# Kernel optimization log

Measured on AMD Instinct MI355X. Metric: run time of the kernel, lower is better.

The kernel has to match this reference:

```python
import jax, jax.numpy as jnp
import numpy as np

E, K, H, I = 16, 4, 2048, 1024
B, S = 1, 2048


def setup_inputs() -> dict:
    key = jax.random.key(0)
    ks = jax.random.split(key, 5)
    scale_in = 1.0 / np.sqrt(H)
    scale_mid = 1.0 / np.sqrt(I)
    return {
        "x": jax.random.normal(ks[0], (B, S, H), dtype=jnp.float32),
        "gate_w": jax.random.normal(ks[1], (E, H), dtype=jnp.float32) * scale_in,
        "w1_gate": jax.random.normal(ks[2], (E, I, H), dtype=jnp.float32) * scale_in,
        "w1_up": jax.random.normal(ks[3], (E, I, H), dtype=jnp.float32) * scale_in,
        "w2": jax.random.normal(ks[4], (E, H, I), dtype=jnp.float32) * scale_mid,
        "topk": K,
    }


def reference(x, gate_w, w1_gate, w1_up, w2, topk):
    orig_shape = x.shape
    xt = x.reshape(-1, x.shape[-1])            # [T, H]
    T = xt.shape[0]
    n_exp = gate_w.shape[0]

    # Router: top-k logits, softmax over the selected k (as in the torch code).
    logits = xt @ gate_w.T                      # [T, E]
    topk_vals, topk_ids = jax.lax.top_k(logits, topk)
    topk_w = jax.nn.softmax(topk_vals, axis=-1)  # [T, K]

    # Dense per-token-per-expert combine weight; 0 for unselected experts.
    # Mathematically identical to the gather/scatter-add loop: unselected
    # experts contribute expert_out * 0.
    gate_dense = jnp.zeros((T, n_exp), dtype=xt.dtype)
    gate_dense = gate_dense.at[jnp.arange(T)[:, None], topk_ids].add(topk_w)

    # SwiGLU per expert (dense over experts; weights zero-out unused ones).
    g = jnp.einsum("th,eih->tei", xt, w1_gate)   # [T, E, I]
    u = jnp.einsum("th,eih->tei", xt, w1_up)     # [T, E, I]
    h = jax.nn.silu(g) * u                        # [T, E, I]
    out = jnp.einsum("tei,te,ehi->th", h, gate_dense, w2)  # [T, H]
    return out.reshape(orig_shape)
```

## Files before the change

### kernel.cpp

```cpp
#include <hip/hip_runtime.h>
#include <hip/hip_bf16.h>
#include <stdint.h>

#define NEXP 16
#define KSEL 4
#define HDIM 2048
#define IDIM 1024
#define TTOK 2048
#define MAXTILES 80
#define NTA 8
#define NTB 16
#define MAXBA (MAXTILES * NTA)
#define MAXBB (MAXTILES * NTB)
#define NCVT 1024
#define NW8 ((NEXP * IDIM * HDIM) / 8)

typedef __attribute__((ext_vector_type(8))) short bf16x8;
typedef __attribute__((ext_vector_type(4))) float f32x4;
typedef __attribute__((ext_vector_type(4))) unsigned int u32x4;
typedef unsigned int u32;

__device__ __forceinline__ uint32_t pack2(float a, float b) {
  __hip_bfloat162 h = __float22bfloat162_rn(float2{a, b});
  uint32_t u;
  __builtin_memcpy(&u, &h, 4);
  return u;
}
__device__ __forceinline__ ushort bf1(float a) {
  __hip_bfloat16 h = __float2bfloat16(a);
  ushort u;
  __builtin_memcpy(&u, &h, 2);
  return u;
}
__device__ __forceinline__ float bf2f(ushort u) {
  uint32_t v = (uint32_t)u << 16;
  float f;
  __builtin_memcpy(&f, &v, 4);
  return f;
}
__device__ __forceinline__ void gload16(const void* g, void* l) {
  __builtin_amdgcn_global_load_lds(
      (const __attribute__((address_space(1))) u32*)g,
      (__attribute__((address_space(3))) u32*)l, 16, 0, 0);
}
__device__ __forceinline__ int swzread(int row, int q) {
  return row * 32 + ((q ^ ((row >> 1) & 3)) << 3);
}
__device__ __forceinline__ void cvt_body(const float* __restrict__ src,
                                         ushort* __restrict__ dst,
                                         int blk, int nblk) {
  const int stride = nblk * 256;
  for (int i = blk * 256 + (int)threadIdx.x; i < NW8; i += stride) {
    f32x4 a = __builtin_nontemporal_load(((const f32x4*)src) + i * 2);
    f32x4 b = __builtin_nontemporal_load(((const f32x4*)src) + i * 2 + 1);
    uint4 t;
    t.x = pack2(a[0], a[1]); t.y = pack2(a[2], a[3]);
    t.z = pack2(b[0], b[1]); t.w = pack2(b[2], b[3]);
    ((uint4*)dst)[i] = t;
  }
}

__global__ __launch_bounds__(256) void router_kernel(
    const float* __restrict__ x, const float* __restrict__ gw,
    ushort* __restrict__ xb, int* __restrict__ topk_id,
    float* __restrict__ topk_w,
    const float* __restrict__ srcG, ushort* __restrict__ dstG,
    const float* __restrict__ srcU, ushort* __restrict__ dstU)
{
  if (blockIdx.x >= TTOK / 4 + NCVT) {
    cvt_body(srcU, dstU, blockIdx.x - (TTOK / 4 + NCVT), NCVT);
    return;
  }
  if (blockIdx.x >= TTOK / 4) {
    cvt_body(srcG, dstG, blockIdx.x - TTOK / 4, NCVT);
    return;
  }
  const int wid = threadIdx.x >> 6;
  const int lane = threadIdx.x & 63;
  const int t = blockIdx.x * 4 + wid;
  const float4* x4 = (const float4*)(x + (size_t)t * HDIM);
  const float4* gw4 = (const float4*)gw;
  float acc[NEXP];
#pragma unroll
  for (int e = 0; e < NEXP; ++e) acc[e] = 0.f;
#pragma unroll
  for (int i = 0; i < HDIM / 256; ++i) {
    const int idx = i * 64 + lane;
    float4 xv = x4[idx];
    uint2 xp;
    xp.x = pack2(xv.x, xv.y);
    xp.y = pack2(xv.z, xv.w);
    *(uint2*)(xb + (size_t)t * HDIM + idx * 4) = xp;
#pragma unroll
    for (int e = 0; e < NEXP; ++e) {
      float4 wv = gw4[e * (HDIM / 4) + idx];
      acc[e] += xv.x * wv.x + xv.y * wv.y + xv.z * wv.z + xv.w * wv.w;
    }
  }
#pragma unroll
  for (int e = 0; e < NEXP; ++e) {
#pragma unroll
    for (int off = 32; off >= 1; off >>= 1)
      acc[e] += __shfl_xor(acc[e], off);
  }
  if (lane == 0) {
    unsigned taken = 0;
    float vals[KSEL];
    int ids[KSEL];
#pragma unroll
    for (int k = 0; k < KSEL; ++k) {
      float bv = -3.4e38f; int bi = 0;
      for (int e = 0; e < NEXP; ++e)
        if (!((taken >> e) & 1u) && acc[e] > bv) { bv = acc[e]; bi = e; }
      taken |= 1u << bi; vals[k] = bv; ids[k] = bi;
    }
    float m = vals[0], s = 0.f, w[KSEL];
#pragma unroll
    for (int k = 0; k < KSEL; ++k) { w[k] = __expf(vals[k] - m); s += w[k]; }
    float is = 1.f / s;
#pragma unroll
    for (int k = 0; k < KSEL; ++k) {
      topk_id[t * KSEL + k] = ids[k];
      topk_w[t * KSEL + k] = w[k] * is;
    }
  }
}

__global__ __launch_bounds__(1024) void plan_scatter_kernel(
    const int* __restrict__ topk_id, int* __restrict__ counts,
    int* __restrict__ offsets, int* __restrict__ nWA, int* __restrict__ nWB,
    int* __restrict__ wlA, int* __restrict__ wlB,
    int* __restrict__ rowTok, int* __restrict__ inv)
{
  __shared__ int cnt[NEXP], off[NEXP], cur[NEXP], tiles[NEXP], pre[NEXP];
  const int tid = threadIdx.x;
  if (tid < NEXP) { cnt[tid] = 0; cur[tid] = 0; }
  __syncthreads();
  for (int i = tid; i < TTOK * KSEL; i += 1024)
    atomicAdd(&cnt[topk_id[i]], 1);
  __syncthreads();
  if (tid == 0) {
    int s = 0, p = 0;
    for (int e = 0; e < NEXP; ++e) {
      off[e] = s; s += cnt[e];
      tiles[e] = (cnt[e] + 127) >> 7;
      pre[e] = p; p += tiles[e];
    }
    *nWA = p * NTA;
    *nWB = p * NTB;
  }
  __syncthreads();
  if (tid < NEXP) {
    counts[tid] = cnt[tid];
    offsets[tid] = off[tid];
    const int e = tid, T = tiles[e];
    int idx = pre[e] * NTA;
    for (int nt = 0; nt < NTA; ++nt)
      for (int mt = 0; mt < T; ++mt)
        wlA[idx++] = (e << 12) | (nt << 6) | mt;
  } else if (tid < 2 * NEXP) {
    const int e = tid - NEXP, T = tiles[e];
    int idx = pre[e] * NTB;
    for (int nt = 0; nt < NTB; ++nt)
      for (int mt = 0; mt < T; ++mt)
        wlB[idx++] = (e << 12) | (nt << 6) | mt;
  }
  for (int i = tid; i < TTOK * KSEL; i += 1024) {
    const int e = topk_id[i];
    const int pos = atomicAdd(&cur[e], 1);
    const int row = off[e] + pos;
    rowTok[row] = i >> 2;
    inv[i] = row;
  }
}

__global__ __launch_bounds__(256) void gemmA_kernel(
    const ushort* __restrict__ xb,
    const ushort* __restrict__ wG, ushort* __restrict__ gbuf,
    const ushort* __restrict__ wU, ushort* __restrict__ ubuf,
    const int* __restrict__ rowTok, const int* __restrict__ counts,
    const int* __restrict__ offsets, const int* __restrict__ nW,
    const int* __restrict__ wl,
    const float* __restrict__ cvsrc, ushort* __restrict__ cvdst)
{
  int bid = blockIdx.x;
  if (bid >= 2 * MAXBA) {
    cvt_body(cvsrc, cvdst, bid - 2 * MAXBA, NCVT);
    return;
  }
  const ushort* wb;
  ushort* outb;
  if (bid >= MAXBA) { wb = wU; outb = ubuf; bid -= MAXBA; }
  else              { wb = wG; outb = gbuf; }

  const int nTot = *nW;
  const int L = (bid & 7) * (MAXBA / 8) + (bid >> 3);
  if (L >= nTot) return;
  const int w = wl[L];
  const int e = w >> 12, nt = (w >> 6) & 63, mt = w & 63;
  const int n_e = counts[e], rowbase = offsets[e];

  __shared__ ushort As[2][128 * 32];
  __shared__ ushort Bs[2][128 * 32];

  const int tid = threadIdx.x;
  const int r0 = tid >> 2;
  const int ck = tid & 3;
  const int sch = (ck ^ ((r0 >> 1) & 3)) << 3;

  const int ar0 = mt * 128 + r0, ar1 = ar0 + 64;
  const int tok0 = rowTok[rowbase + (ar0 < n_e ? ar0 : n_e - 1)];
  const int tok1 = rowTok[rowbase + (ar1 < n_e ? ar1 : n_e - 1)];
  const ushort* pA0 = xb + (size_t)tok0 * HDIM + sch;
  const ushort* pA1 = xb + (size_t)tok1 * HDIM + sch;
  const size_t wbase = (size_t)e * IDIM * HDIM;
  const ushort* pB0 = wb + wbase + (size_t)(nt * 128 + r0) * HDIM + sch;
  const ushort* pB1 = wb + wbase + (size_t)(nt * 128 + r0 + 64) * HDIM + sch;

  const int lane = tid & 63;
  const int wid = tid >> 6;
  const int wr = (wid >> 1) << 6;
  const int wc = (wid & 1) << 6;
  const int lr = lane & 15;
  const int q = lane >> 4;

  f32x4 acc[4][4];
#pragma unroll
  for (int i = 0; i < 4; ++i)
#pragma unroll
    for (int j = 0; j < 4; ++j) acc[i][j] = (f32x4){0.f, 0.f, 0.f, 0.f};

  auto STAGE = [&](int b) {
    gload16(pA0, &As[b][tid * 8]);
    gload16(pA1, &As[b][2048 + tid * 8]);
    gload16(pB0, &Bs[b][tid * 8]);
    gload16(pB1, &Bs[b][2048 + tid * 8]);
    pA0 += 32; pA1 += 32; pB0 += 32; pB1 += 32;
  };

  const int NTK = HDIM / 32;
  STAGE(0);
  __syncthreads();
  int buf = 0;
  for (int kt = 0; kt < NTK; ++kt) {
    if (kt + 1 < NTK) STAGE(buf ^ 1);
    bf16x8 af[4], bfr[4];
#pragma unroll
    for (int mi = 0; mi < 4; ++mi)
      af[mi] = *(const bf16x8*)&As[buf][swzread(wr + mi * 16 + lr, q)];
#pragma unroll
    for (int ni = 0; ni < 4; ++ni)
      bfr[ni] = *(const bf16x8*)&Bs[buf][swzread(wc + ni * 16 + lr, q)];
#pragma unroll
    for (int mi = 0; mi < 4; ++mi)
#pragma unroll
      for (int ni = 0; ni < 4; ++ni)
        acc[mi][ni] = __builtin_amdgcn_mfma_f32_16x16x32_bf16(af[mi], bfr[ni], acc[mi][ni], 0, 0, 0);
    __syncthreads();
    buf ^= 1;
  }

#pragma unroll
  for (int mi = 0; mi < 4; ++mi) {
#pragma unroll
    for (int ni = 0; ni < 4; ++ni) {
      const int col = nt * 128 + wc + ni * 16 + lr;
#pragma unroll
      for (int r = 0; r < 4; ++r) {
        const int mrow = mt * 128 + wr + mi * 16 + q * 4 + r;
        if (mrow < n_e)
          outb[(size_t)(rowbase + mrow) * IDIM + col] = bf1(acc[mi][ni][r]);
      }
    }
  }
}

__global__ __launch_bounds__(256) void gemmB_kernel(
    const ushort* __restrict__ hb, const ushort* __restrict__ wb,
    const int* __restrict__ counts, const int* __restrict__ offsets,
    const int* __restrict__ nW, const int* __restrict__ wl,
    ushort* __restrict__ po)
{
  const int nTot = *nW;
  const int L = (blockIdx.x & 7) * (MAXBB / 8) + (blockIdx.x >> 3);
  if (L >= nTot) return;
  const int w = wl[L];
  const int e = w >> 12, nt = (w >> 6) & 63, mt = w & 63;
  const int n_e = counts[e], rowbase = offsets[e];

  __shared__ ushort As[2][128 * 32];
  __shared__ ushort Bs[2][128 * 32];

  const int tid = threadIdx.x;
  const int r0 = tid >> 2;
  const int ck = tid & 3;
  const int sch = (ck ^ ((r0 >> 1) & 3)) << 3;

  const int ar0 = mt * 128 + r0, ar1 = ar0 + 64;
  const int g0 = rowbase + (ar0 < n_e ? ar0 : n_e - 1);
  const int g1 = rowbase + (ar1 < n_e ? ar1 : n_e - 1);
  const ushort* pA0 = hb + (size_t)g0 * IDIM + sch;
  const ushort* pA1 = hb + (size_t)g1 * IDIM + sch;
  const size_t wbase = (size_t)e * HDIM * IDIM;
  const ushort* pB0 = wb + wbase + (size_t)(nt * 128 + r0) * IDIM + sch;
  const ushort* pB1 = wb + wbase + (size_t)(nt * 128 + r0 + 64) * IDIM + sch;

  const int lane = tid & 63;
  const int wid = tid >> 6;
  const int wr = (wid >> 1) << 6;
  const int wc = (wid & 1) << 6;
  const int lr = lane & 15;
  const int q = lane >> 4;

  f32x4 acc[4][4];
#pragma unroll
  for (int i = 0; i < 4; ++i)
#pragma unroll
    for (int j = 0; j < 4; ++j) acc[i][j] = (f32x4){0.f, 0.f, 0.f, 0.f};

  auto STAGE = [&](int b) {
    gload16(pA0, &As[b][tid * 8]);
    gload16(pA1, &As[b][2048 + tid * 8]);
    gload16(pB0, &Bs[b][tid * 8]);
    gload16(pB1, &Bs[b][2048 + tid * 8]);
    pA0 += 32; pA1 += 32; pB0 += 32; pB1 += 32;
  };

  const int NTK = IDIM / 32;
  STAGE(0);
  __syncthreads();
  int buf = 0;
  for (int kt = 0; kt < NTK; ++kt) {
    if (kt + 1 < NTK) STAGE(buf ^ 1);
    bf16x8 af[4], bfr[4];
#pragma unroll
    for (int mi = 0; mi < 4; ++mi)
      af[mi] = *(const bf16x8*)&As[buf][swzread(wr + mi * 16 + lr, q)];
#pragma unroll
    for (int ni = 0; ni < 4; ++ni)
      bfr[ni] = *(const bf16x8*)&Bs[buf][swzread(wc + ni * 16 + lr, q)];
#pragma unroll
    for (int mi = 0; mi < 4; ++mi)
#pragma unroll
      for (int ni = 0; ni < 4; ++ni)
        acc[mi][ni] = __builtin_amdgcn_mfma_f32_16x16x32_bf16(af[mi], bfr[ni], acc[mi][ni], 0, 0, 0);
    __syncthreads();
    buf ^= 1;
  }

#pragma unroll
  for (int mi = 0; mi < 4; ++mi) {
#pragma unroll
    for (int ni = 0; ni < 4; ++ni) {
      const int col = nt * 128 + wc + ni * 16 + lr;
#pragma unroll
      for (int r = 0; r < 4; ++r) {
        const int mrow = mt * 128 + wr + mi * 16 + q * 4 + r;
        if (mrow < n_e)
          po[(size_t)(rowbase + mrow) * HDIM + col] = bf1(acc[mi][ni][r]);
      }
    }
  }
}

__global__ __launch_bounds__(256) void silu_kernel(
    const ushort* __restrict__ g, const ushort* __restrict__ u,
    ushort* __restrict__ h, int n8)
{
  const int stride = gridDim.x * 256;
  for (int i = blockIdx.x * 256 + threadIdx.x; i < n8; i += stride) {
    u32x4 gv = __builtin_nontemporal_load(((const u32x4*)g) + i);
    u32x4 uv = __builtin_nontemporal_load(((const u32x4*)u) + i);
    uint4 hv;
#pragma unroll
    for (int wd = 0; wd < 4; ++wd) {
      const uint32_t gw2 = gv[wd], uw2 = uv[wd];
      const float g0 = bf2f((ushort)(gw2 & 0xffff));
      const float g1 = bf2f((ushort)(gw2 >> 16));
      const float u0 = bf2f((ushort)(uw2 & 0xffff));
      const float u1 = bf2f((ushort)(uw2 >> 16));
      const float h0 = (g0 / (1.f + __expf(-g0))) * u0;
      const float h1 = (g1 / (1.f + __expf(-g1))) * u1;
      (&hv.x)[wd] = pack2(h0, h1);
    }
    ((uint4*)h)[i] = hv;
  }
}

__global__ __launch_bounds__(256) void combine_kernel(
    const ushort* __restrict__ po, const int* __restrict__ inv,
    const float* __restrict__ tw, float* __restrict__ out)
{
  const int t = blockIdx.x;
  const int r0 = inv[t * 4 + 0], r1 = inv[t * 4 + 1];
  const int r2 = inv[t * 4 + 2], r3 = inv[t * 4 + 3];
  const float w0 = tw[t * 4 + 0], w1 = tw[t * 4 + 1];
  const float w2v = tw[t * 4 + 2], w3 = tw[t * 4 + 3];
  const int i = threadIdx.x;
  uint4 v0 = *(const uint4*)(po + (size_t)r0 * HDIM + i * 8);
  uint4 v1 = *(const uint4*)(po + (size_t)r1 * HDIM + i * 8);
  uint4 v2 = *(const uint4*)(po + (size_t)r2 * HDIM + i * 8);
  uint4 v3 = *(const uint4*)(po + (size_t)r3 * HDIM + i * 8);
  float o[8];
#pragma unroll
  for (int w = 0; w < 4; ++w) {
    const uint32_t a = (&v0.x)[w], b = (&v1.x)[w], c = (&v2.x)[w], d = (&v3.x)[w];
    o[w * 2 + 0] = w0 * __builtin_bit_cast(float, a << 16) +
                   w1 * __builtin_bit_cast(float, b << 16) +
                   w2v * __builtin_bit_cast(float, c << 16) +
                   w3 * __builtin_bit_cast(float, d << 16);
    o[w * 2 + 1] = w0 * __builtin_bit_cast(float, a & 0xffff0000u) +
                   w1 * __builtin_bit_cast(float, b & 0xffff0000u) +
                   w2v * __builtin_bit_cast(float, c & 0xffff0000u) +
                   w3 * __builtin_bit_cast(float, d & 0xffff0000u);
  }
  float4* o4 = (float4*)(out + (size_t)t * HDIM + i * 8);
  o4[0] = (float4){o[0], o[1], o[2], o[3]};
  o4[1] = (float4){o[4], o[5], o[6], o[7]};
}

extern "C" void kernel_launch(void* const* d_in, const int* in_sizes, int n_in,
                              void* d_out, int out_size, void* d_ws, size_t ws_size,
                              hipStream_t stream) {
  const float* x   = (const float*)d_in[0];
  const float* gw  = (const float*)d_in[1];
  const float* w1g = (const float*)d_in[2];
  const float* w1u = (const float*)d_in[3];
  const float* w2  = (const float*)d_in[4];
  float* out = (float*)d_out;

  char* ws = (char*)d_ws;
  ushort* xb    = (ushort*)(ws + 0);
  ushort* wbufG = (ushort*)(ws + 8388608);
  ushort* wbufU = (ushort*)(ws + 75497472);
  ushort* wbuf2 = (ushort*)(ws + 142606336);
  ushort* gbuf  = (ushort*)(ws + 209715200);
  ushort* ubuf  = (ushort*)(ws + 226492416);
  ushort* hbuf  = (ushort*)(ws + 243269632);
  ushort* po    = (ushort*)(ws + 260046848);
  int*    tkid   = (int*)(ws + 293601280);
  float*  tkw    = (float*)(ws + 293601280 + 32768);
  int*    rowTok = (int*)(ws + 293601280 + 65536);
  int*    inv    = (int*)(ws + 293601280 + 98304);
  int*    ctrl   = (int*)(ws + 293732352);
  int* counts  = ctrl;
  int* offsets = ctrl + 32;
  int* nWA     = ctrl + 50;
  int* nWB     = ctrl + 51;
  int* wlA     = ctrl + 64;
  int* wlB     = ctrl + 64 + MAXBA;

  router_kernel<<<TTOK / 4 + 2 * NCVT, 256, 0, stream>>>(
      x, gw, xb, tkid, tkw, w1g, wbufG, w1u, wbufU);
  plan_scatter_kernel<<<1, 1024, 0, stream>>>(tkid, counts, offsets, nWA, nWB,
                                              wlA, wlB, rowTok, inv);
  gemmA_kernel<<<2 * MAXBA + NCVT, 256, 0, stream>>>(
      xb, wbufG, gbuf, wbufU, ubuf, rowTok, counts, offsets, nWA, wlA,
      w2, wbuf2);
  silu_kernel<<<2048, 256, 0, stream>>>(gbuf, ubuf, hbuf, (TTOK * KSEL * IDIM) / 8);
  gemmB_kernel<<<MAXBB, 256, 0, stream>>>(hbuf, wbuf2, counts, offsets,
                                          nWB, wlB, po);
  combine_kernel<<<TTOK, 256, 0, stream>>>(po, inv, tkw, out);
}
```

Before: 327.0 us.

## Split gemmA reduction dimension in two and sum fp32 partials in SiLU kernel

The first grouped GEMM now splits the H reduction into two halves, doubling the number of workgroups. Each half writes fp32 partial results to separate buffers, and the SiLU kernel adds the partials before applying the activation. This aims to improve occupancy and load balance across CUs for the gate/up projection. In exchange it writes and reads four fp32 intermediates instead of two bf16 ones, which is several times more memory traffic.

```diff
diff --git a/kernel.cpp b/kernel.cpp
--- a/kernel.cpp
+++ b/kernel.cpp
@@ -176,22 +176,24 @@
 
 __global__ __launch_bounds__(256) void gemmA_kernel(
     const ushort* __restrict__ xb,
-    const ushort* __restrict__ wG, ushort* __restrict__ gbuf,
-    const ushort* __restrict__ wU, ushort* __restrict__ ubuf,
+    const ushort* __restrict__ wG, const ushort* __restrict__ wU,
+    float* __restrict__ gp0, float* __restrict__ gp1,
+    float* __restrict__ up0, float* __restrict__ up1,
     const int* __restrict__ rowTok, const int* __restrict__ counts,
     const int* __restrict__ offsets, const int* __restrict__ nW,
     const int* __restrict__ wl,
     const float* __restrict__ cvsrc, ushort* __restrict__ cvdst)
 {
   int bid = blockIdx.x;
-  if (bid >= 2 * MAXBA) {
-    cvt_body(cvsrc, cvdst, bid - 2 * MAXBA, NCVT);
+  if (bid >= 4 * MAXBA) {
+    cvt_body(cvsrc, cvdst, bid - 4 * MAXBA, NCVT);
     return;
   }
-  const ushort* wb;
-  ushort* outb;
-  if (bid >= MAXBA) { wb = wU; outb = ubuf; bid -= MAXBA; }
-  else              { wb = wG; outb = gbuf; }
+  const int seg = bid / MAXBA;
+  bid -= seg * MAXBA;
+  const int kh = seg & 1;
+  const ushort* wb = (seg >> 1) ? wU : wG;
+  float* outp = (seg == 0) ? gp0 : (seg == 1) ? gp1 : (seg == 2) ? up0 : up1;
 
   const int nTot = *nW;
   const int L = (bid & 7) * (MAXBA / 8) + (bid >> 3);
@@ -207,15 +209,16 @@
   const int r0 = tid >> 2;
   const int ck = tid & 3;
   const int sch = (ck ^ ((r0 >> 1) & 3)) << 3;
+  const int kbase = kh * (HDIM / 2);
 
   const int ar0 = mt * 128 + r0, ar1 = ar0 + 64;
   const int tok0 = rowTok[rowbase + (ar0 < n_e ? ar0 : n_e - 1)];
   const int tok1 = rowTok[rowbase + (ar1 < n_e ? ar1 : n_e - 1)];
-  const ushort* pA0 = xb + (size_t)tok0 * HDIM + sch;
-  const ushort* pA1 = xb + (size_t)tok1 * HDIM + sch;
+  const ushort* pA0 = xb + (size_t)tok0 * HDIM + kbase + sch;
+  const ushort* pA1 = xb + (size_t)tok1 * HDIM + kbase + sch;
   const size_t wbase = (size_t)e * IDIM * HDIM;
-  const ushort* pB0 = wb + wbase + (size_t)(nt * 128 + r0) * HDIM + sch;
-  const ushort* pB1 = wb + wbase + (size_t)(nt * 128 + r0 + 64) * HDIM + sch;
+  const ushort* pB0 = wb + wbase + (size_t)(nt * 128 + r0) * HDIM + kbase + sch;
+  const ushort* pB1 = wb + wbase + (size_t)(nt * 128 + r0 + 64) * HDIM + kbase + sch;
 
   const int lane = tid & 63;
   const int wid = tid >> 6;
@@ -238,7 +241,7 @@
     pA0 += 32; pA1 += 32; pB0 += 32; pB1 += 32;
   };
 
-  const int NTK = HDIM / 32;
+  const int NTK = HDIM / 64;
   STAGE(0);
   __syncthreads();
   int buf = 0;
@@ -269,7 +272,7 @@
       for (int r = 0; r < 4; ++r) {
         const int mrow = mt * 128 + wr + mi * 16 + q * 4 + r;
         if (mrow < n_e)
-          outb[(size_t)(rowbase + mrow) * IDIM + col] = bf1(acc[mi][ni][r]);
+          outp[(size_t)(rowbase + mrow) * IDIM + col] = acc[mi][ni][r];
       }
     }
   }
@@ -364,26 +367,28 @@
 }
 
 __global__ __launch_bounds__(256) void silu_kernel(
-    const ushort* __restrict__ g, const ushort* __restrict__ u,
-    ushort* __restrict__ h, int n8)
+    const float* __restrict__ g0p, const float* __restrict__ g1p,
+    const float* __restrict__ u0p, const float* __restrict__ u1p,
+    ushort* __restrict__ h, int n4)
 {
   const int stride = gridDim.x * 256;
-  for (int i = blockIdx.x * 256 + threadIdx.x; i < n8; i += stride) {
-    u32x4 gv = __builtin_nontemporal_load(((const u32x4*)g) + i);
-    u32x4 uv = __builtin_nontemporal_load(((const u32x4*)u) + i);
-    uint4 hv;
-#pragma unroll
-    for (int wd = 0; wd < 4; ++wd) {
-      const uint32_t gw2 = gv[wd], uw2 = uv[wd];
-      const float g0 = bf2f((ushort)(gw2 & 0xffff));
-      const float g1 = bf2f((ushort)(gw2 >> 16));
-      const float u0 = bf2f((ushort)(uw2 & 0xffff));
-      const float u1 = bf2f((ushort)(uw2 >> 16));
-      const float h0 = (g0 / (1.f + __expf(-g0))) * u0;
-      const float h1 = (g1 / (1.f + __expf(-g1))) * u1;
+  for (int i = blockIdx.x * 256 + threadIdx.x; i < n4; i += stride) {
+    f32x4 a = __builtin_nontemporal_load(((const f32x4*)g0p) + i);
+    f32x4 b = __builtin_nontemporal_load(((const f32x4*)g1p) + i);
+    f32x4 c = __builtin_nontemporal_load(((const f32x4*)u0p) + i);
+    f32x4 d = __builtin_nontemporal_load(((const f32x4*)u1p) + i);
+    uint2 hv;
+#pragma unroll
+    for (int wd = 0; wd < 2; ++wd) {
+      const float ga = a[wd * 2] + b[wd * 2];
+      const float gb = a[wd * 2 + 1] + b[wd * 2 + 1];
+      const float ua = c[wd * 2] + d[wd * 2];
+      const float ub = c[wd * 2 + 1] + d[wd * 2 + 1];
+      const float h0 = (ga / (1.f + __expf(-ga))) * ua;
+      const float h1 = (gb / (1.f + __expf(-gb))) * ub;
       (&hv.x)[wd] = pack2(h0, h1);
     }
-    ((uint4*)h)[i] = hv;
+    ((uint2*)h)[i] = hv;
   }
 }
 
@@ -434,15 +439,17 @@
   ushort* wbufG = (ushort*)(ws + 8388608);
   ushort* wbufU = (ushort*)(ws + 75497472);
   ushort* wbuf2 = (ushort*)(ws + 142606336);
-  ushort* gbuf  = (ushort*)(ws + 209715200);
-  ushort* ubuf  = (ushort*)(ws + 226492416);
-  ushort* hbuf  = (ushort*)(ws + 243269632);
-  ushort* po    = (ushort*)(ws + 260046848);
-  int*    tkid   = (int*)(ws + 293601280);
-  float*  tkw    = (float*)(ws + 293601280 + 32768);
-  int*    rowTok = (int*)(ws + 293601280 + 65536);
-  int*    inv    = (int*)(ws + 293601280 + 98304);
-  int*    ctrl   = (int*)(ws + 293732352);
+  float*  gp0   = (float*) (ws + 209715200);
+  float*  gp1   = (float*) (ws + 243269632);
+  float*  up0   = (float*) (ws + 276824064);
+  float*  up1   = (float*) (ws + 310378496);
+  ushort* hbuf  = (ushort*)(ws + 343932928);
+  ushort* po    = (ushort*)(ws + 360710144);
+  int*    tkid   = (int*)(ws + 394264576);
+  float*  tkw    = (float*)(ws + 394264576 + 32768);
+  int*    rowTok = (int*)(ws + 394264576 + 65536);
+  int*    inv    = (int*)(ws + 394264576 + 98304);
+  int*    ctrl   = (int*)(ws + 394395648);
   int* counts  = ctrl;
   int* offsets = ctrl + 32;
   int* nWA     = ctrl + 50;
@@ -454,10 +461,11 @@
       x, gw, xb, tkid, tkw, w1g, wbufG, w1u, wbufU);
   plan_scatter_kernel<<<1, 1024, 0, stream>>>(tkid, counts, offsets, nWA, nWB,
                                               wlA, wlB, rowTok, inv);
-  gemmA_kernel<<<2 * MAXBA + NCVT, 256, 0, stream>>>(
-      xb, wbufG, gbuf, wbufU, ubuf, rowTok, counts, offsets, nWA, wlA,
+  gemmA_kernel<<<4 * MAXBA + NCVT, 256, 0, stream>>>(
+      xb, wbufG, wbufU, gp0, gp1, up0, up1, rowTok, counts, offsets, nWA, wlA,
       w2, wbuf2);
-  silu_kernel<<<2048, 256, 0, stream>>>(gbuf, ubuf, hbuf, (TTOK * KSEL * IDIM) / 8);
+  silu_kernel<<<2048, 256, 0, stream>>>(gp0, gp1, up0, up1, hbuf,
+                                        (TTOK * KSEL * IDIM) / 4);
   gemmB_kernel<<<MAXBB, 256, 0, stream>>>(hbuf, wbuf2, counts, offsets,
                                           nWB, wlB, po);
   combine_kernel<<<TTOK, 256, 0, stream>>>(po, inv, tkw, out);
```

New measurement: 363.2 us. 1.11x slower.

## Fuse gate/up GEMMs with SiLU epilogue and drop separate silu kernel

Applied to the files above, without the earlier changes.

The first grouped GEMM now computes gate and up projections together in one block, with each block covering 64 output columns of both weights, and applies SiLU(g)*u in the epilogue before writing h directly. This removes the gbuf/ubuf round trip through global memory, the separate elementwise kernel, and one launch. Each A tile is now loaded once for both projections instead of twice. The cost is a narrower N tile per weight and twice as many accumulators per block. The gate value is also no longer rounded to bf16 before the activation.

```diff
diff --git a/kernel.cpp b/kernel.cpp
--- a/kernel.cpp
+++ b/kernel.cpp
@@ -8,9 +8,9 @@
 #define IDIM 1024
 #define TTOK 2048
 #define MAXTILES 80
-#define NTA 8
+#define NT1 16
 #define NTB 16
-#define MAXBA (MAXTILES * NTA)
+#define MAXB1 (MAXTILES * NT1)
 #define MAXBB (MAXTILES * NTB)
 #define NCVT 1024
 #define NW8 ((NEXP * IDIM * HDIM) / 8)
@@ -146,7 +146,7 @@
       tiles[e] = (cnt[e] + 127) >> 7;
       pre[e] = p; p += tiles[e];
     }
-    *nWA = p * NTA;
+    *nWA = p * NT1;
     *nWB = p * NTB;
   }
   __syncthreads();
@@ -154,8 +154,8 @@
     counts[tid] = cnt[tid];
     offsets[tid] = off[tid];
     const int e = tid, T = tiles[e];
-    int idx = pre[e] * NTA;
-    for (int nt = 0; nt < NTA; ++nt)
+    int idx = pre[e] * NT1;
+    for (int nt = 0; nt < NT1; ++nt)
       for (int mt = 0; mt < T; ++mt)
         wlA[idx++] = (e << 12) | (nt << 6) | mt;
   } else if (tid < 2 * NEXP) {
@@ -174,34 +174,28 @@
   }
 }
 
-__global__ __launch_bounds__(256) void gemmA_kernel(
+__global__ __launch_bounds__(256) void gemm1_kernel(
     const ushort* __restrict__ xb,
-    const ushort* __restrict__ wG, ushort* __restrict__ gbuf,
-    const ushort* __restrict__ wU, ushort* __restrict__ ubuf,
+    const ushort* __restrict__ wG, const ushort* __restrict__ wU,
     const int* __restrict__ rowTok, const int* __restrict__ counts,
     const int* __restrict__ offsets, const int* __restrict__ nW,
-    const int* __restrict__ wl,
+    const int* __restrict__ wl, ushort* __restrict__ hbuf,
     const float* __restrict__ cvsrc, ushort* __restrict__ cvdst)
 {
-  int bid = blockIdx.x;
-  if (bid >= 2 * MAXBA) {
-    cvt_body(cvsrc, cvdst, bid - 2 * MAXBA, NCVT);
+  if (blockIdx.x >= MAXB1) {
+    cvt_body(cvsrc, cvdst, blockIdx.x - MAXB1, NCVT);
     return;
   }
-  const ushort* wb;
-  ushort* outb;
-  if (bid >= MAXBA) { wb = wU; outb = ubuf; bid -= MAXBA; }
-  else              { wb = wG; outb = gbuf; }
-
   const int nTot = *nW;
-  const int L = (bid & 7) * (MAXBA / 8) + (bid >> 3);
+  const int L = (blockIdx.x & 7) * (MAXB1 / 8) + (blockIdx.x >> 3);
   if (L >= nTot) return;
   const int w = wl[L];
   const int e = w >> 12, nt = (w >> 6) & 63, mt = w & 63;
   const int n_e = counts[e], rowbase = offsets[e];
 
   __shared__ ushort As[2][128 * 32];
-  __shared__ ushort Bs[2][128 * 32];
+  __shared__ ushort Bg[2][64 * 32];
+  __shared__ ushort Bu[2][64 * 32];
 
   const int tid = threadIdx.x;
   const int r0 = tid >> 2;
@@ -214,28 +208,31 @@
   const ushort* pA0 = xb + (size_t)tok0 * HDIM + sch;
   const ushort* pA1 = xb + (size_t)tok1 * HDIM + sch;
   const size_t wbase = (size_t)e * IDIM * HDIM;
-  const ushort* pB0 = wb + wbase + (size_t)(nt * 128 + r0) * HDIM + sch;
-  const ushort* pB1 = wb + wbase + (size_t)(nt * 128 + r0 + 64) * HDIM + sch;
+  const ushort* pBg = wG + wbase + (size_t)(nt * 64 + r0) * HDIM + sch;
+  const ushort* pBu = wU + wbase + (size_t)(nt * 64 + r0) * HDIM + sch;
 
   const int lane = tid & 63;
   const int wid = tid >> 6;
   const int wr = (wid >> 1) << 6;
-  const int wc = (wid & 1) << 6;
+  const int wc = (wid & 1) << 5;
   const int lr = lane & 15;
   const int q = lane >> 4;
 
-  f32x4 acc[4][4];
+  f32x4 accG[4][2], accU[4][2];
 #pragma unroll
   for (int i = 0; i < 4; ++i)
 #pragma unroll
-    for (int j = 0; j < 4; ++j) acc[i][j] = (f32x4){0.f, 0.f, 0.f, 0.f};
+    for (int j = 0; j < 2; ++j) {
+      accG[i][j] = (f32x4){0.f, 0.f, 0.f, 0.f};
+      accU[i][j] = (f32x4){0.f, 0.f, 0.f, 0.f};
+    }
 
   auto STAGE = [&](int b) {
     gload16(pA0, &As[b][tid * 8]);
     gload16(pA1, &As[b][2048 + tid * 8]);
-    gload16(pB0, &Bs[b][tid * 8]);
-    gload16(pB1, &Bs[b][2048 + tid * 8]);
-    pA0 += 32; pA1 += 32; pB0 += 32; pB1 += 32;
+    gload16(pBg, &Bg[b][tid * 8]);
+    gload16(pBu, &Bu[b][tid * 8]);
+    pA0 += 32; pA1 += 32; pBg += 32; pBu += 32;
   };
 
   const int NTK = HDIM / 32;
@@ -244,18 +241,22 @@
   int buf = 0;
   for (int kt = 0; kt < NTK; ++kt) {
     if (kt + 1 < NTK) STAGE(buf ^ 1);
-    bf16x8 af[4], bfr[4];
+    bf16x8 af[4], bg[2], bu[2];
 #pragma unroll
     for (int mi = 0; mi < 4; ++mi)
       af[mi] = *(const bf16x8*)&As[buf][swzread(wr + mi * 16 + lr, q)];
 #pragma unroll
-    for (int ni = 0; ni < 4; ++ni)
-      bfr[ni] = *(const bf16x8*)&Bs[buf][swzread(wc + ni * 16 + lr, q)];
+    for (int ni = 0; ni < 2; ++ni) {
+      bg[ni] = *(const bf16x8*)&Bg[buf][swzread(wc + ni * 16 + lr, q)];
+      bu[ni] = *(const bf16x8*)&Bu[buf][swzread(wc + ni * 16 + lr, q)];
+    }
 #pragma unroll
     for (int mi = 0; mi < 4; ++mi)
 #pragma unroll
-      for (int ni = 0; ni < 4; ++ni)
-        acc[mi][ni] = __builtin_amdgcn_mfma_f32_16x16x32_bf16(af[mi], bfr[ni], acc[mi][ni], 0, 0, 0);
+      for (int ni = 0; ni < 2; ++ni) {
+        accG[mi][ni] = __builtin_amdgcn_mfma_f32_16x16x32_bf16(af[mi], bg[ni], accG[mi][ni], 0, 0, 0);
+        accU[mi][ni] = __builtin_amdgcn_mfma_f32_16x16x32_bf16(af[mi], bu[ni], accU[mi][ni], 0, 0, 0);
+      }
     __syncthreads();
     buf ^= 1;
   }
@@ -263,13 +264,17 @@
 #pragma unroll
   for (int mi = 0; mi < 4; ++mi) {
 #pragma unroll
-    for (int ni = 0; ni < 4; ++ni) {
-      const int col = nt * 128 + wc + ni * 16 + lr;
+    for (int ni = 0; ni < 2; ++ni) {
+      const int col = nt * 64 + wc + ni * 16 + lr;
 #pragma unroll
       for (int r = 0; r < 4; ++r) {
         const int mrow = mt * 128 + wr + mi * 16 + q * 4 + r;
-        if (mrow < n_e)
-          outb[(size_t)(rowbase + mrow) * IDIM + col] = bf1(acc[mi][ni][r]);
+        if (mrow < n_e) {
+          const float gv = accG[mi][ni][r];
+          const float uv = accU[mi][ni][r];
+          const float hv = (gv / (1.f + __expf(-gv))) * uv;
+          hbuf[(size_t)(rowbase + mrow) * IDIM + col] = bf1(hv);
+        }
       }
     }
   }
@@ -360,30 +365,6 @@
           po[(size_t)(rowbase + mrow) * HDIM + col] = bf1(acc[mi][ni][r]);
       }
     }
-  }
-}
-
-__global__ __launch_bounds__(256) void silu_kernel(
-    const ushort* __restrict__ g, const ushort* __restrict__ u,
-    ushort* __restrict__ h, int n8)
-{
-  const int stride = gridDim.x * 256;
-  for (int i = blockIdx.x * 256 + threadIdx.x; i < n8; i += stride) {
-    u32x4 gv = __builtin_nontemporal_load(((const u32x4*)g) + i);
-    u32x4 uv = __builtin_nontemporal_load(((const u32x4*)u) + i);
-    uint4 hv;
-#pragma unroll
-    for (int wd = 0; wd < 4; ++wd) {
-      const uint32_t gw2 = gv[wd], uw2 = uv[wd];
-      const float g0 = bf2f((ushort)(gw2 & 0xffff));
-      const float g1 = bf2f((ushort)(gw2 >> 16));
-      const float u0 = bf2f((ushort)(uw2 & 0xffff));
-      const float u1 = bf2f((ushort)(uw2 >> 16));
-      const float h0 = (g0 / (1.f + __expf(-g0))) * u0;
-      const float h1 = (g1 / (1.f + __expf(-g1))) * u1;
-      (&hv.x)[wd] = pack2(h0, h1);
-    }
-    ((uint4*)h)[i] = hv;
   }
 }
 
@@ -434,30 +415,27 @@
   ushort* wbufG = (ushort*)(ws + 8388608);
   ushort* wbufU = (ushort*)(ws + 75497472);
   ushort* wbuf2 = (ushort*)(ws + 142606336);
-  ushort* gbuf  = (ushort*)(ws + 209715200);
-  ushort* ubuf  = (ushort*)(ws + 226492416);
-  ushort* hbuf  = (ushort*)(ws + 243269632);
-  ushort* po    = (ushort*)(ws + 260046848);
-  int*    tkid   = (int*)(ws + 293601280);
-  float*  tkw    = (float*)(ws + 293601280 + 32768);
-  int*    rowTok = (int*)(ws + 293601280 + 65536);
-  int*    inv    = (int*)(ws + 293601280 + 98304);
-  int*    ctrl   = (int*)(ws + 293732352);
+  ushort* hbuf  = (ushort*)(ws + 209715200);
+  ushort* po    = (ushort*)(ws + 226492416);
+  int*    tkid   = (int*)(ws + 260046848);
+  float*  tkw    = (float*)(ws + 260046848 + 32768);
+  int*    rowTok = (int*)(ws + 260046848 + 65536);
+  int*    inv    = (int*)(ws + 260046848 + 98304);
+  int*    ctrl   = (int*)(ws + 260177920);
   int* counts  = ctrl;
   int* offsets = ctrl + 32;
   int* nWA     = ctrl + 50;
   int* nWB     = ctrl + 51;
   int* wlA     = ctrl + 64;
-  int* wlB     = ctrl + 64 + MAXBA;
+  int* wlB     = ctrl + 64 + MAXB1;
 
   router_kernel<<<TTOK / 4 + 2 * NCVT, 256, 0, stream>>>(
       x, gw, xb, tkid, tkw, w1g, wbufG, w1u, wbufU);
   plan_scatter_kernel<<<1, 1024, 0, stream>>>(tkid, counts, offsets, nWA, nWB,
                                               wlA, wlB, rowTok, inv);
-  gemmA_kernel<<<2 * MAXBA + NCVT, 256, 0, stream>>>(
-      xb, wbufG, gbuf, wbufU, ubuf, rowTok, counts, offsets, nWA, wlA,
+  gemm1_kernel<<<MAXB1 + NCVT, 256, 0, stream>>>(
+      xb, wbufG, wbufU, rowTok, counts, offsets, nWA, wlA, hbuf,
       w2, wbuf2);
-  silu_kernel<<<2048, 256, 0, stream>>>(gbuf, ubuf, hbuf, (TTOK * KSEL * IDIM) / 8);
   gemmB_kernel<<<MAXBB, 256, 0, stream>>>(hbuf, wbuf2, counts, offsets,
                                           nWB, wlB, po);
   combine_kernel<<<TTOK, 256, 0, stream>>>(po, inv, tkw, out);
```

New measurement: 326.3 us. Within noise of the previous version (-0.2%).
